# Performance work log

Measured on AMD Instinct MI355X. Metric: run time of the kernel, lower is better.

Reference implementation:

```python
import jax, jax.numpy as jnp
import numpy as np

B, C, D = 8192, 1000, 2048
CLAMP_MIN, CLAMP_MAX = 1e-12, 1e12
SEP_WEIGHT = 0.001


def setup_inputs() -> dict:
    key = jax.random.key(0)
    k1, k2, k3 = jax.random.split(key, 3)
    x = jax.random.normal(k1, (B, D), dtype=jnp.float32)
    centers = jax.random.normal(k2, (C, D), dtype=jnp.float32)
    labels = jax.random.randint(k3, (B,), 0, C, dtype=jnp.int64)
    return {"x": x, "centers": centers, "labels": labels}


def reference(x, centers, labels):
    distmat = (
        jnp.sum(x * x, axis=1, keepdims=True)
        + jnp.sum(centers * centers, axis=1)[None, :]
        - 2.0 * (x @ centers.T)
    )
    d = jnp.clip(distmat, CLAMP_MIN, CLAMP_MAX)
    mask = labels[:, None] == jnp.arange(C, dtype=labels.dtype)[None, :]  # [B, C]
    bsz = x.shape[0]
    ncls = centers.shape[0]
    # each row has exactly one True in mask -> counts are B and B*(C-1)
    center_loss = jnp.sum(jnp.where(mask, d, 0.0)) / bsz
    sep_loss = jnp.sum(jnp.where(mask, 0.0, d)) / (bsz * (ncls - 1))
    return center_loss - SEP_WEIGHT * sep_loss
```

## Files before the change

### kernel.cpp

```cpp
#include <hip/hip_runtime.h>


#define DD 2048
#define NB 8192
#define NC 1000
#define D4 (DD / 4)
#define THREADS 256
#define XROWS 8
#define XBLOCKS (NB / XROWS)
#define CTILES 8
#define CRG 8
#define CBLOCKS (CTILES * CRG)

#define CQ_OFF   0
#define CSQ_OFF  65536
#define PART_OFF 65792

__device__ __forceinline__ float dot4(float4 a, float4 b) {
    return a.x * b.x + a.y * b.y + a.z * b.z + a.w * b.w;
}
__device__ __forceinline__ void acc4(float4& a, float4 b) {
    a.x += b.x; a.y += b.y; a.z += b.z; a.w += b.w;
}

__global__ __launch_bounds__(THREADS) void centers_kernel(
        const float4* __restrict__ c4, float4* __restrict__ cq,
        float* __restrict__ csq_part) {
    const int t = threadIdx.x;
    const int tile = blockIdx.x & (CTILES - 1);
    const int rg = blockIdx.x >> 3;
    const int col4 = tile * 64 + (t & 63);
    const int rlane = t >> 6;
    const int row0 = rg * 125;

    float4 acc = make_float4(0.f, 0.f, 0.f, 0.f);
    float csq = 0.f;
    for (int r = rlane; r < 125; r += 4) {
        float4 v = c4[(size_t)(row0 + r) * D4 + col4];
        acc4(acc, v);
        csq += dot4(v, v);
    }

    __shared__ float4 lds[4][64];
    lds[rlane][t & 63] = acc;
    __syncthreads();
    if (t < 64) {
        float4 s = lds[0][t];
        acc4(s, lds[1][t]); acc4(s, lds[2][t]); acc4(s, lds[3][t]);
        cq[rg * 512 + tile * 64 + t] = s;
    }

    __shared__ float red[THREADS / 64];
    for (int off = 32; off > 0; off >>= 1) csq += __shfl_down(csq, off, 64);
    const int lane = t & 63, wv = t >> 6;
    if (lane == 0) red[wv] = csq;
    __syncthreads();
    if (t == 0)
        csq_part[blockIdx.x] = red[0] + red[1] + red[2] + red[3];
}

__global__ __launch_bounds__(THREADS) void x_kernel(
        const float4* __restrict__ x4, const float4* __restrict__ c4,
        const int* __restrict__ labels, const float4* __restrict__ cq,
        float4* __restrict__ partials) {
    const int t = threadIdx.x;
    const int b = blockIdx.x;

    float4 sc0 = make_float4(0.f, 0.f, 0.f, 0.f);
    float4 sc1 = make_float4(0.f, 0.f, 0.f, 0.f);
#pragma unroll
    for (int r = 0; r < CRG; ++r) {
        acc4(sc0, cq[r * 512 + t]);
        acc4(sc1, cq[r * 512 + 256 + t]);
    }

    const int rows0 = b * XROWS;
    int labs[XROWS];
#pragma unroll
    for (int r = 0; r < XROWS; ++r) labs[r] = labels[rows0 + r];

    const float4* xr = x4 + (size_t)rows0 * D4 + t;
    float sx = 0.f, sdot = 0.f, scl = 0.f, s2 = 0.f;

    float4 xa = xr[0], xb = xr[256];
    const float4* cr = c4 + (size_t)labs[0] * D4 + t;
    float4 ca = cr[0], cb = cr[256];
#pragma unroll
    for (int r = 0; r < XROWS; ++r) {
        float4 nxa, nxb, nca, ncb;
        if (r + 1 < XROWS) {
            nxa = xr[(r + 1) * D4];
            nxb = xr[(r + 1) * D4 + 256];
            const float4* np = c4 + (size_t)labs[r + 1] * D4 + t;
            nca = np[0];
            ncb = np[256];
        }
        sx   += dot4(xa, xa) + dot4(xb, xb);
        sdot += dot4(xa, ca) + dot4(xb, cb);
        scl  += dot4(ca, ca) + dot4(cb, cb);
        s2   += dot4(xa, sc0) + dot4(xb, sc1);
        if (r + 1 < XROWS) { xa = nxa; xb = nxb; ca = nca; cb = ncb; }
    }

    __shared__ float red[4][THREADS / 64];
    for (int off = 32; off > 0; off >>= 1) {
        sx   += __shfl_down(sx, off, 64);
        sdot += __shfl_down(sdot, off, 64);
        scl  += __shfl_down(scl, off, 64);
        s2   += __shfl_down(s2, off, 64);
    }
    const int lane = t & 63, wv = t >> 6;
    if (lane == 0) {
        red[0][wv] = sx; red[1][wv] = sdot;
        red[2][wv] = scl; red[3][wv] = s2;
    }
    __syncthreads();
    if (t == 0) {
        float4 s;
        s.x = red[0][0] + red[0][1] + red[0][2] + red[0][3];
        s.y = red[1][0] + red[1][1] + red[1][2] + red[1][3];
        s.z = red[2][0] + red[2][1] + red[2][2] + red[2][3];
        s.w = red[3][0] + red[3][1] + red[3][2] + red[3][3];
        partials[b] = s;
    }
}

__global__ __launch_bounds__(THREADS) void finalize_kernel(
        const float4* __restrict__ partials, const float* __restrict__ csq_part,
        float* __restrict__ out) {
    const int t = threadIdx.x;

    double sx = 0.0, sdot = 0.0, scl = 0.0, s2 = 0.0, csq = 0.0;
    for (int i = t; i < XBLOCKS; i += THREADS) {
        float4 p = partials[i];
        sx += (double)p.x; sdot += (double)p.y;
        scl += (double)p.z; s2 += (double)p.w;
    }
    if (t < CBLOCKS) csq = (double)csq_part[t];

    __shared__ double red[5][THREADS / 64];
    for (int off = 32; off > 0; off >>= 1) {
        sx   += __shfl_down(sx, off, 64);
        sdot += __shfl_down(sdot, off, 64);
        scl  += __shfl_down(scl, off, 64);
        s2   += __shfl_down(s2, off, 64);
        csq  += __shfl_down(csq, off, 64);
    }
    const int lane = t & 63, wv = t >> 6;
    if (lane == 0) {
        red[0][wv] = sx; red[1][wv] = sdot; red[2][wv] = scl;
        red[3][wv] = s2; red[4][wv] = csq;
    }
    __syncthreads();
    if (t == 0) {
        double Sx   = red[0][0] + red[0][1] + red[0][2] + red[0][3];
        double Sdot = red[1][0] + red[1][1] + red[1][2] + red[1][3];
        double Scl  = red[2][0] + red[2][1] + red[2][2] + red[2][3];
        double S2   = red[3][0] + red[3][1] + red[3][2] + red[3][3];
        double Sc   = red[4][0] + red[4][1] + red[4][2] + red[4][3];
        double sum_all  = (double)NC * Sx + (double)NB * Sc - 2.0 * S2;
        double sum_diag = Sx + Scl - 2.0 * Sdot;
        double center_loss = sum_diag / (double)NB;
        double sep_loss =
            (sum_all - sum_diag) / ((double)NB * (double)(NC - 1));
        out[0] = (float)(center_loss - 0.001 * sep_loss);
    }
}

extern "C" void kernel_launch(void* const* d_in, const int* in_sizes, int n_in,
                              void* d_out, int out_size, void* d_ws, size_t ws_size,
                              hipStream_t stream) {
    const float4* x4 = (const float4*)d_in[0];
    const float4* c4 = (const float4*)d_in[1];
    const int* labels = (const int*)d_in[2];

    float4* cq = (float4*)((char*)d_ws + CQ_OFF);
    float* csq_part = (float*)((char*)d_ws + CSQ_OFF);
    float4* partials = (float4*)((char*)d_ws + PART_OFF);
    float* out = (float*)d_out;

    centers_kernel<<<CBLOCKS, THREADS, 0, stream>>>(c4, cq, csq_part);
    x_kernel<<<XBLOCKS, THREADS, 0, stream>>>(x4, c4, labels,
                                              (const float4*)cq, partials);
    finalize_kernel<<<1, THREADS, 0, stream>>>(partials, csq_part, out);
}
```

Measured before the change: 117.2 us.

## Split x rows across two blocks per half-dimension and pre-fold center sums

```diff
diff --git a/kernel.cpp b/kernel.cpp
--- a/kernel.cpp
+++ b/kernel.cpp
@@ -5,16 +5,18 @@
 #define NB 8192
 #define NC 1000
 #define D4 (DD / 4)
+#define HALF4 256
 #define THREADS 256
 #define XROWS 8
-#define XBLOCKS (NB / XROWS)
+#define XBLOCKS ((NB / XROWS) * 2)
 #define CTILES 8
 #define CRG 8
 #define CBLOCKS (CTILES * CRG)
 
 #define CQ_OFF   0
-#define CSQ_OFF  65536
-#define PART_OFF 65792
+#define SC_OFF   65536
+#define CSQ_OFF  73728
+#define PART_OFF 73984
 
 __device__ __forceinline__ float dot4(float4 a, float4 b) {
     return a.x * b.x + a.y * b.y + a.z * b.z + a.w * b.w;
@@ -35,6 +37,7 @@
 
     float4 acc = make_float4(0.f, 0.f, 0.f, 0.f);
     float csq = 0.f;
+#pragma unroll 4
     for (int r = rlane; r < 125; r += 4) {
         float4 v = c4[(size_t)(row0 + r) * D4 + col4];
         acc4(acc, v);
@@ -59,47 +62,51 @@
         csq_part[blockIdx.x] = red[0] + red[1] + red[2] + red[3];
 }
 
+__global__ __launch_bounds__(THREADS) void sc_fold_kernel(
+        const float4* __restrict__ cq, float4* __restrict__ sc4) {
+    const int idx = blockIdx.x * THREADS + threadIdx.x;
+    float4 s = cq[idx];
+#pragma unroll
+    for (int r = 1; r < CRG; ++r) acc4(s, cq[r * 512 + idx]);
+    sc4[idx] = s;
+}
+
 __global__ __launch_bounds__(THREADS) void x_kernel(
         const float4* __restrict__ x4, const float4* __restrict__ c4,
-        const int* __restrict__ labels, const float4* __restrict__ cq,
+        const int* __restrict__ labels, const float4* __restrict__ sc4,
         float4* __restrict__ partials) {
     const int t = threadIdx.x;
     const int b = blockIdx.x;
+    const int rowgrp = b >> 1;
+    const int h = (b & 1) * HALF4;
+    const int rows0 = rowgrp * XROWS;
 
-    float4 sc0 = make_float4(0.f, 0.f, 0.f, 0.f);
-    float4 sc1 = make_float4(0.f, 0.f, 0.f, 0.f);
-#pragma unroll
-    for (int r = 0; r < CRG; ++r) {
-        acc4(sc0, cq[r * 512 + t]);
-        acc4(sc1, cq[r * 512 + 256 + t]);
-    }
+    const float4 sc = sc4[h + t];
 
-    const int rows0 = b * XROWS;
     int labs[XROWS];
 #pragma unroll
     for (int r = 0; r < XROWS; ++r) labs[r] = labels[rows0 + r];
 
-    const float4* xr = x4 + (size_t)rows0 * D4 + t;
+    const float4* xr = x4 + (size_t)rows0 * D4 + h + t;
+    const float4* cbase = c4 + h + t;
+
     float sx = 0.f, sdot = 0.f, scl = 0.f, s2 = 0.f;
 
-    float4 xa = xr[0], xb = xr[256];
-    const float4* cr = c4 + (size_t)labs[0] * D4 + t;
-    float4 ca = cr[0], cb = cr[256];
+    float4 xa = xr[0],      ca = cbase[(size_t)labs[0] * D4];
+    float4 xb = xr[D4],     cb = cbase[(size_t)labs[1] * D4];
 #pragma unroll
     for (int r = 0; r < XROWS; ++r) {
-        float4 nxa, nxb, nca, ncb;
-        if (r + 1 < XROWS) {
-            nxa = xr[(r + 1) * D4];
-            nxb = xr[(r + 1) * D4 + 256];
-            const float4* np = c4 + (size_t)labs[r + 1] * D4 + t;
-            nca = np[0];
-            ncb = np[256];
+        float4 nx, nc;
+        if (r + 2 < XROWS) {
+            nx = xr[(size_t)(r + 2) * D4];
+            nc = cbase[(size_t)labs[r + 2] * D4];
         }
-        sx   += dot4(xa, xa) + dot4(xb, xb);
-        sdot += dot4(xa, ca) + dot4(xb, cb);
-        scl  += dot4(ca, ca) + dot4(cb, cb);
-        s2   += dot4(xa, sc0) + dot4(xb, sc1);
-        if (r + 1 < XROWS) { xa = nxa; xb = nxb; ca = nca; cb = ncb; }
+        sx   += dot4(xa, xa);
+        sdot += dot4(xa, ca);
+        scl  += dot4(ca, ca);
+        s2   += dot4(xa, sc);
+        xa = xb; ca = cb;
+        if (r + 2 < XROWS) { xb = nx; cb = nc; }
     }
 
     __shared__ float red[4][THREADS / 64];
@@ -175,12 +182,14 @@
     const int* labels = (const int*)d_in[2];
 
     float4* cq = (float4*)((char*)d_ws + CQ_OFF);
+    float4* sc = (float4*)((char*)d_ws + SC_OFF);
     float* csq_part = (float*)((char*)d_ws + CSQ_OFF);
     float4* partials = (float4*)((char*)d_ws + PART_OFF);
     float* out = (float*)d_out;
 
     centers_kernel<<<CBLOCKS, THREADS, 0, stream>>>(c4, cq, csq_part);
+    sc_fold_kernel<<<2, THREADS, 0, stream>>>((const float4*)cq, sc);
     x_kernel<<<XBLOCKS, THREADS, 0, stream>>>(x4, c4, labels,
-                                              (const float4*)cq, partials);
+                                              (const float4*)sc, partials);
     finalize_kernel<<<1, THREADS, 0, stream>>>(partials, csq_part, out);
 }
```

Result: faster. 111.0 us (-5.3%).
